# Optimization experiments

Measured on AMD Instinct MI355X. Metric: run time of the kernel, lower is better.

The kernel has to match this reference:

```python
import jax, jax.numpy as jnp
import numpy as np

N_NODES = 100000


def gcn_conv(x, W, b, src, dst):
    """PyG-style GCNConv: symmetric normalization with self-loops.
    x: [N, Cin], W: [Cin, Cout], b: [Cout], src/dst: [E] int (messages src->dst)."""
    N = x.shape[0]
    h = x @ W  # [N, Cout]
    # degree with self-loops (fill_value = 1)
    deg = jnp.ones((N,), dtype=x.dtype).at[dst].add(1.0)
    d_inv = jax.lax.rsqrt(deg)
    norm = d_inv[src] * d_inv[dst]  # [E]
    msg = h[src] * norm[:, None]  # [E, Cout] -- dominant memory traffic
    agg = jnp.zeros_like(h).at[dst].add(msg)
    # self-loop contribution: norm_ii = d_inv[i]^2
    agg = agg + h * (d_inv * d_inv)[:, None]
    return agg + b


def setup_inputs() -> dict:
    key = jax.random.key(0)
    k1, k2, k3, k4 = jax.random.split(key, 4)
    N, E, Cin, Chid, Cout = N_NODES, 1600000, 128, 128, 64
    x = jax.random.normal(k1, (N, Cin), dtype=jnp.float32)
    edge_index = jax.random.randint(k2, (2, E), 0, N, dtype=jnp.int32)
    W1 = jax.random.normal(k3, (Cin, Chid), dtype=jnp.float32) / np.sqrt(Cin)
    b1 = jnp.zeros((Chid,), dtype=jnp.float32)
    W2 = jax.random.normal(k4, (Chid, Cout), dtype=jnp.float32) / np.sqrt(Chid)
    b2 = jnp.zeros((Cout,), dtype=jnp.float32)
    return {"x": x, "edge_index": edge_index, "W1": W1, "b1": b1, "W2": W2, "b2": b2}


def reference(x, edge_index, W1, b1, W2, b2):
    src, dst = edge_index[0], edge_index[1]
    h = jax.nn.relu(gcn_conv(x, W1, b1, src, dst))  # conv1: in -> 2*out
    z = jax.nn.relu(gcn_conv(h, W2, b2, src, dst))  # conv2: 2*out -> out
    return z
```

## Files before the change

### kernel.cpp

```cpp
#include <hip/hip_runtime.h>
#include <hip/hip_fp16.h>

#define TPB 256
#define CAP 32
#define OVFCAP 65536

typedef __attribute__((ext_vector_type(8))) short bf16x8;
typedef __attribute__((ext_vector_type(4))) float f32x4;

__device__ inline void split1(float x, unsigned short& h, unsigned short& l) {
  unsigned xb = __float_as_uint(x);
  h = (unsigned short)(xb >> 16);
  float hf = __uint_as_float(xb & 0xFFFF0000u);
  float lf = x - hf;
  l = (unsigned short)(__float_as_uint(lf) >> 16);
}

__device__ inline void split4(const float4 v, ushort4& h, ushort4& l) {
  split1(v.x, h.x, l.x);
  split1(v.y, h.y, l.y);
  split1(v.z, h.z, l.z);
  split1(v.w, h.w, l.w);
}

__global__ void k_fillslot(const int* __restrict__ src, const int* __restrict__ dst,
                           int* __restrict__ cnt, int* __restrict__ col2,
                           uint2* __restrict__ ovf, int* __restrict__ ovfn,
                           int E, int N) {
  const int g = blockIdx.x & 7;
  const int gb = blockIdx.x >> 3;
  const int gstride = (gridDim.x >> 3) * blockDim.x;
  const int lo = (int)(((long long)g * N) >> 3);
  const int hi = (int)(((long long)(g + 1) * N) >> 3);
  for (int e = gb * blockDim.x + threadIdx.x; e < E; e += gstride) {
    int d = __builtin_nontemporal_load(dst + e);
    if (d >= lo && d < hi) {
      int s = __builtin_nontemporal_load(src + e);
      int c = atomicAdd(cnt + d, 1);
      if (c < CAP) {
        col2[(size_t)d * CAP + c] = s;
      } else {
        int p = atomicAdd(ovfn, 1);
        if (p < OVFCAP) ovf[p] = make_uint2((unsigned)d, (unsigned)s);
      }
    }
  }
}

__global__ void k_dinv_from_cnt(const int* __restrict__ cnt, float* __restrict__ dinv, int N) {
  int i = blockIdx.x * blockDim.x + threadIdx.x;
  if (i < N) dinv[i] = rsqrtf((float)(cnt[i] + 1));
}

__global__ void k_prep_wt2(const float* __restrict__ W1, unsigned short* __restrict__ W1h,
                           unsigned short* __restrict__ W1l, int K1, int C1,
                           const float* __restrict__ W2, unsigned short* __restrict__ W2h,
                           unsigned short* __restrict__ W2l, int K2, int C2) {
  int i = blockIdx.x * blockDim.x + threadIdx.x;
  int n1 = K1 * C1;
  if (i < n1) {
    int k = i / C1, c = i % C1;
    unsigned short h, l;
    split1(W1[i], h, l);
    W1h[(size_t)c * K1 + k] = h;
    W1l[(size_t)c * K1 + k] = l;
  } else if (i < n1 + K2 * C2) {
    int ii = i - n1;
    int k = ii / C2, c = ii % C2;
    unsigned short h, l;
    split1(W2[ii], h, l);
    W2h[(size_t)c * K2 + k] = h;
    W2l[(size_t)c * K2 + k] = l;
  }
}

template<int COUT>
__launch_bounds__(512)
__global__ void k_gemm_mfma(const float* __restrict__ X, const unsigned short* __restrict__ Wh,
                            const unsigned short* __restrict__ Wl, const float* __restrict__ dinv,
                            __half* __restrict__ Y16, int N) {
  constexpr int K = 128;
  constexpr int BM = 128;
  constexpr int WCOL = COUT / 2;
  constexpr int NFRAG = WCOL / 16;
  __shared__ unsigned short Ah[BM * K], Al[BM * K];
  __shared__ unsigned short Wsh[COUT * K], Wsl[COUT * K];

  const int tid = threadIdx.x;
  const int rb = blockIdx.x * BM;

  {
    const uint4* gh = (const uint4*)Wh;
    const uint4* gl = (const uint4*)Wl;
    for (int i = tid; i < COUT * 16; i += 512) {
      int r = i >> 4, c = i & 15;
      int byte = r * 256 + ((c * 16) ^ ((r & 7) << 4));
      *(uint4*)((char*)Wsh + byte) = gh[i];
      *(uint4*)((char*)Wsl + byte) = gl[i];
    }
  }
  {
    for (int i = tid; i < BM * 32; i += 512) {
      int r = i >> 5, c4 = i & 31;
      int g = rb + r;
      if (g < N) {
        float4 v = ((const float4*)(X + (size_t)g * K))[c4];
        ushort4 h, l;
        split4(v, h, l);
        int byte = r * 256 + ((c4 * 8) ^ ((r & 7) << 4));
        *(ushort4*)((char*)Ah + byte) = h;
        *(ushort4*)((char*)Al + byte) = l;
      }
    }
  }
  __syncthreads();

  const int wid = tid >> 6, lane = tid & 63;
  const int wm = wid & 3;
  const int wn = wid >> 2;
  const int RB = wm * 32;
  const int CB = wn * WCOL;
  const int l15 = lane & 15, l4 = lane >> 4;
  const int xs = (l15 & 7) << 4;

  f32x4 acc[2][NFRAG];
  #pragma unroll
  for (int m = 0; m < 2; ++m)
    #pragma unroll
    for (int n = 0; n < NFRAG; ++n)
      acc[m][n] = (f32x4){0.f, 0.f, 0.f, 0.f};

  #pragma unroll
  for (int ks = 0; ks < 4; ++ks) {
    const int cbx = (ks * 64 + l4 * 16) ^ xs;
    bf16x8 a0h = *(const bf16x8*)((const char*)Ah + (RB + l15) * 256 + cbx);
    bf16x8 a0l = *(const bf16x8*)((const char*)Al + (RB + l15) * 256 + cbx);
    bf16x8 a1h = *(const bf16x8*)((const char*)Ah + (RB + 16 + l15) * 256 + cbx);
    bf16x8 a1l = *(const bf16x8*)((const char*)Al + (RB + 16 + l15) * 256 + cbx);
    #pragma unroll
    for (int n = 0; n < NFRAG; ++n) {
      const int wr = CB + n * 16 + l15;
      bf16x8 bh = *(const bf16x8*)((const char*)Wsh + wr * 256 + cbx);
      bf16x8 bl = *(const bf16x8*)((const char*)Wsl + wr * 256 + cbx);
      acc[0][n] = __builtin_amdgcn_mfma_f32_16x16x32_bf16(a0h, bh, acc[0][n], 0, 0, 0);
      acc[0][n] = __builtin_amdgcn_mfma_f32_16x16x32_bf16(a0h, bl, acc[0][n], 0, 0, 0);
      acc[0][n] = __builtin_amdgcn_mfma_f32_16x16x32_bf16(a0l, bh, acc[0][n], 0, 0, 0);
      acc[1][n] = __builtin_amdgcn_mfma_f32_16x16x32_bf16(a1h, bh, acc[1][n], 0, 0, 0);
      acc[1][n] = __builtin_amdgcn_mfma_f32_16x16x32_bf16(a1h, bl, acc[1][n], 0, 0, 0);
      acc[1][n] = __builtin_amdgcn_mfma_f32_16x16x32_bf16(a1l, bh, acc[1][n], 0, 0, 0);
    }
  }

  #pragma unroll
  for (int m = 0; m < 2; ++m) {
    #pragma unroll
    for (int q = 0; q < 4; ++q) {
      int row = rb + RB + m * 16 + l4 * 4 + q;
      if (row < N) {
        float dv = dinv[row];
        __half* yr = Y16 + (size_t)row * COUT + CB + l15;
        #pragma unroll
        for (int n = 0; n < NFRAG; ++n) yr[n * 16] = __float2half(acc[m][n][q] * dv);
      }
    }
  }
}

template<int C>
__launch_bounds__(256)
__global__ void k_aggv(const __half* __restrict__ hsh, const float* __restrict__ dinv,
                       const int* __restrict__ cnt, const int* __restrict__ col2,
                       const uint2* __restrict__ ovf, const int* __restrict__ ovfn,
                       const float* __restrict__ bias, float* __restrict__ out, int N) {
  constexpr int LPR = C / 8;
  constexpr int NG = 64 / LPR;
  constexpr int SPR = 4 * NG;
  constexpr int NR = CAP / SPR;
  const int node = blockIdx.x * 4 + (threadIdx.x >> 6);
  if (node >= N) return;
  const int lane = threadIdx.x & 63;
  const int i = lane % LPR;
  const int j = lane / LPR;
  const int deg = cnt[node];
  const int m = min(deg, CAP);
  const int4* cp4 = (const int4*)(col2 + (size_t)node * CAP);
  const size_t coloff = (size_t)i * 8;

  float acc[8];
  #pragma unroll
  for (int q = 0; q < 8; ++q) acc[q] = 0.f;

  #pragma unroll
  for (int r = 0; r < NR; ++r) {
    if (r * SPR < m) {
      int4 idx = cp4[r * NG + j];
      int s0 = r * SPR + 4 * j;
      bool ok0 = s0 + 0 < m, ok1 = s0 + 1 < m, ok2 = s0 + 2 < m, ok3 = s0 + 3 < m;
      int n0 = ok0 ? idx.x : 0;
      int n1 = ok1 ? idx.y : 0;
      int n2 = ok2 ? idx.z : 0;
      int n3 = ok3 ? idx.w : 0;
      uint4 v0 = *(const uint4*)((const char*)hsh + ((size_t)n0 * C + coloff) * 2);
      uint4 v1 = *(const uint4*)((const char*)hsh + ((size_t)n1 * C + coloff) * 2);
      uint4 v2 = *(const uint4*)((const char*)hsh + ((size_t)n2 * C + coloff) * 2);
      uint4 v3 = *(const uint4*)((const char*)hsh + ((size_t)n3 * C + coloff) * 2);
      float f0 = ok0 ? 1.f : 0.f, f1 = ok1 ? 1.f : 0.f;
      float f2 = ok2 ? 1.f : 0.f, f3 = ok3 ? 1.f : 0.f;
      const __half2* h0 = (const __half2*)&v0;
      const __half2* h1 = (const __half2*)&v1;
      const __half2* h2 = (const __half2*)&v2;
      const __half2* h3 = (const __half2*)&v3;
      #pragma unroll
      for (int q = 0; q < 4; ++q) {
        float2 a = __half22float2(h0[q]);
        float2 b = __half22float2(h1[q]);
        float2 c = __half22float2(h2[q]);
        float2 d = __half22float2(h3[q]);
        acc[2 * q]     = fmaf(f0, a.x, acc[2 * q]);
        acc[2 * q + 1] = fmaf(f0, a.y, acc[2 * q + 1]);
        acc[2 * q]     = fmaf(f1, b.x, acc[2 * q]);
        acc[2 * q + 1] = fmaf(f1, b.y, acc[2 * q + 1]);
        acc[2 * q]     = fmaf(f2, c.x, acc[2 * q]);
        acc[2 * q + 1] = fmaf(f2, c.y, acc[2 * q + 1]);
        acc[2 * q]     = fmaf(f3, d.x, acc[2 * q]);
        acc[2 * q + 1] = fmaf(f3, d.y, acc[2 * q + 1]);
      }
    }
  }

  if (deg > CAP && j == 0) {
    int on = min(*ovfn, (int)OVFCAP);
    for (int k = 0; k < on; ++k) {
      uint2 eo = ovf[k];
      if ((int)eo.x == node) {
        uint4 v = *(const uint4*)((const char*)hsh + ((size_t)eo.y * C + coloff) * 2);
        const __half2* h2 = (const __half2*)&v;
        #pragma unroll
        for (int q = 0; q < 4; ++q) {
          float2 a = __half22float2(h2[q]);
          acc[2 * q] += a.x;
          acc[2 * q + 1] += a.y;
        }
      }
    }
  }

  #pragma unroll
  for (int off = LPR; off < 64; off <<= 1)
    #pragma unroll
    for (int q = 0; q < 8; ++q)
      acc[q] += __shfl_xor(acc[q], off);

  if (j < 2) {
    const float dv = dinv[node];
    const int f4 = 2 * i + j;
    uint2 sh = *(const uint2*)((const char*)hsh + ((size_t)node * C + (size_t)f4 * 4) * 2);
    const __half2* shh = (const __half2*)&sh;
    float2 s01 = __half22float2(shh[0]);
    float2 s23 = __half22float2(shh[1]);
    float4 bb = ((const float4*)bias)[f4];
    float4 o;
    o.x = fmaxf(fmaf(dv, s01.x + acc[4 * j + 0], bb.x), 0.f);
    o.y = fmaxf(fmaf(dv, s01.y + acc[4 * j + 1], bb.y), 0.f);
    o.z = fmaxf(fmaf(dv, s23.x + acc[4 * j + 2], bb.z), 0.f);
    o.w = fmaxf(fmaf(dv, s23.y + acc[4 * j + 3], bb.w), 0.f);
    ((float4*)(out + (size_t)node * C))[f4] = o;
  }
}

__global__ void k_fill1(float* __restrict__ p, int n) {
  int i = blockIdx.x * blockDim.x + threadIdx.x;
  if (i < n) p[i] = 1.0f;
}
__global__ void k_deg_scatter(const int* __restrict__ dst, float* __restrict__ deg, int E) {
  int e = blockIdx.x * blockDim.x + threadIdx.x;
  if (e < E) atomicAdd(deg + dst[e], 1.0f);
}
__global__ void k_rsqrt_inplace(float* __restrict__ p, int n) {
  int i = blockIdx.x * blockDim.x + threadIdx.x;
  if (i < n) p[i] = rsqrtf(p[i]);
}
template<int COUT>
__launch_bounds__(256)
__global__ void k_gemm128(const float* __restrict__ X, const float* __restrict__ W,
                          const float* __restrict__ dinv, float* __restrict__ Y, int N) {
  constexpr int K = 128;
  constexpr int CG = COUT / 8;
  constexpr int ROWS = 256 / CG;
  constexpr int XSTR = K + 4;
  __shared__ float Ws[K * COUT];
  __shared__ float Xs[ROWS * XSTR];
  const int tid = threadIdx.x;

  const float4* W4 = (const float4*)W;
  float4* Ws4 = (float4*)Ws;
  #pragma unroll
  for (int i = tid; i < K * COUT / 4; i += 256) Ws4[i] = W4[i];

  const int rb = blockIdx.x * ROWS;
  float4* Xs4 = (float4*)Xs;
  for (int i = tid; i < ROWS * (K / 4); i += 256) {
    int r = i / (K / 4), c = i % (K / 4);
    float4 v = make_float4(0.f, 0.f, 0.f, 0.f);
    if (rb + r < N) v = ((const float4*)(X + (size_t)(rb + r) * K))[c];
    Xs4[r * (XSTR / 4) + c] = v;
  }
  __syncthreads();

  const int lrow = tid / CG;
  const int cg = tid % CG;
  const int row = rb + lrow;
  float acc[8];
  #pragma unroll
  for (int jj = 0; jj < 8; ++jj) acc[jj] = 0.f;
  const float* xr = Xs + lrow * XSTR;
  #pragma unroll 4
  for (int k = 0; k < K; ++k) {
    float xv = xr[k];
    float4 w0 = Ws4[k * (COUT / 4) + cg * 2];
    float4 w1 = Ws4[k * (COUT / 4) + cg * 2 + 1];
    acc[0] = fmaf(xv, w0.x, acc[0]);
    acc[1] = fmaf(xv, w0.y, acc[1]);
    acc[2] = fmaf(xv, w0.z, acc[2]);
    acc[3] = fmaf(xv, w0.w, acc[3]);
    acc[4] = fmaf(xv, w1.x, acc[4]);
    acc[5] = fmaf(xv, w1.y, acc[5]);
    acc[6] = fmaf(xv, w1.z, acc[6]);
    acc[7] = fmaf(xv, w1.w, acc[7]);
  }
  if (row < N) {
    float ds = dinv[row];
    float4* y = (float4*)(Y + (size_t)row * COUT + cg * 8);
    y[0] = make_float4(acc[0] * ds, acc[1] * ds, acc[2] * ds, acc[3] * ds);
    y[1] = make_float4(acc[4] * ds, acc[5] * ds, acc[6] * ds, acc[7] * ds);
  }
}
template<int C>
__global__ void k_selfinit2(const float* __restrict__ hs, const float* __restrict__ dinv,
                            float* __restrict__ agg, int N) {
  int i = blockIdx.x * blockDim.x + threadIdx.x;
  int total = N * (C / 4);
  if (i >= total) return;
  int node = i / (C / 4);
  float di = dinv[node];
  float4 v = ((const float4*)hs)[i];
  ((float4*)agg)[i] = make_float4(v.x * di, v.y * di, v.z * di, v.w * di);
}
template<int C>
__global__ void k_scatter(const float* __restrict__ hs, const float* __restrict__ dinv,
                          const int* __restrict__ src, const int* __restrict__ dst,
                          float* __restrict__ agg, int E) {
  constexpr int LPE = C / 4;
  long long t = (long long)blockIdx.x * blockDim.x + threadIdx.x;
  int e = (int)(t / LPE);
  if (e >= E) return;
  int c4 = (int)(t % LPE);
  int s = src[e], d = dst[e];
  float nd = dinv[d];
  float4 v = ((const float4*)(hs + (size_t)s * C))[c4];
  float* a = agg + (size_t)d * C + (size_t)c4 * 4;
  atomicAdd(a + 0, v.x * nd);
  atomicAdd(a + 1, v.y * nd);
  atomicAdd(a + 2, v.z * nd);
  atomicAdd(a + 3, v.w * nd);
}
template<int C>
__global__ void k_relu_bias(const float* __restrict__ agg, const float* __restrict__ b,
                            float* __restrict__ out, int N) {
  int i = blockIdx.x * blockDim.x + threadIdx.x;
  int total = N * (C / 4);
  if (i >= total) return;
  int c4 = i % (C / 4);
  float4 bb = ((const float4*)b)[c4];
  float4 v = ((const float4*)agg)[i];
  v.x = fmaxf(v.x + bb.x, 0.f);
  v.y = fmaxf(v.y + bb.y, 0.f);
  v.z = fmaxf(v.z + bb.z, 0.f);
  v.w = fmaxf(v.w + bb.w, 0.f);
  ((float4*)out)[i] = v;
}

extern "C" void kernel_launch(void* const* d_in, const int* in_sizes, int n_in,
                              void* d_out, int out_size, void* d_ws, size_t ws_size,
                              hipStream_t stream) {
  const float* x  = (const float*)d_in[0];
  const int*   ei = (const int*)d_in[1];
  const float* W1 = (const float*)d_in[2];
  const float* b1 = (const float*)d_in[3];
  const float* W2 = (const float*)d_in[4];
  const float* b2 = (const float*)d_in[5];

  const int Cin = 128, Chid = 128, Cout2 = 64;
  const int N = in_sizes[0] / Cin;
  const int E = in_sizes[1] / 2;
  const int* src = ei;
  const int* dst = ei + E;
  float* out = (float*)d_out;
  (void)n_in; (void)out_size;

  const int nbN = (N + TPB - 1) / TPB;
  const int nbE = (E + TPB - 1) / TPB;

  auto align = [](size_t v) { return (v + 511) & ~(size_t)511; };
  char* ws = (char*)d_ws;
  size_t off = 0;
  float* dinv   = (float*)(ws + off); off += align((size_t)N * 4);
  int*   cnt    = (int*)(ws + off);   off += align((size_t)N * 4);
  unsigned short* wt1h = (unsigned short*)(ws + off); off += align((size_t)Cin * Chid * 2);
  unsigned short* wt1l = (unsigned short*)(ws + off); off += align((size_t)Cin * Chid * 2);
  unsigned short* wt2h = (unsigned short*)(ws + off); off += align((size_t)Chid * Cout2 * 2);
  unsigned short* wt2l = (unsigned short*)(ws + off); off += align((size_t)Chid * Cout2 * 2);
  int*   col2   = (int*)(ws + off);   off += align((size_t)N * CAP * 4);
  int*   ovfn   = (int*)(ws + off);   off += align((size_t)64);
  uint2* ovf    = (uint2*)(ws + off); off += align((size_t)OVFCAP * 8);
  float* B      = (float*)(ws + off); off += (size_t)N * Chid * 4;
  __half* H16   = (__half*)(ws + off); off += align((size_t)N * Chid * 2);

  const bool fast_ok = (off <= ws_size);

  if (fast_ok) {
    hipMemsetAsync(cnt, 0, (size_t)N * 4, stream);
    hipMemsetAsync(ovfn, 0, 4, stream);
    k_fillslot<<<4096, TPB, 0, stream>>>(src, dst, cnt, col2, ovf, ovfn, E, N);
    k_dinv_from_cnt<<<nbN, TPB, 0, stream>>>(cnt, dinv, N);

    {
      int total = Cin * Chid + Chid * Cout2;
      k_prep_wt2<<<(total + TPB - 1) / TPB, TPB, 0, stream>>>(
          W1, wt1h, wt1l, Cin, Chid, W2, wt2h, wt2l, Chid, Cout2);
    }

    k_gemm_mfma<128><<<(N + 127) / 128, 512, 0, stream>>>(x, wt1h, wt1l, dinv, H16, N);
    k_aggv<128><<<(N + 3) / 4, 256, 0, stream>>>(H16, dinv, cnt, col2, ovf, ovfn, b1, B, N);
    k_gemm_mfma<64><<<(N + 127) / 128, 512, 0, stream>>>(B, wt2h, wt2l, dinv, H16, N);
    k_aggv<64><<<(N + 3) / 4, 256, 0, stream>>>(H16, dinv, cnt, col2, ovf, ovfn, b2, out, N);
  } else {
    size_t o2 = 0;
    float* dinvF = (float*)(ws + o2); o2 += align((size_t)N * 4);
    float* AF = (float*)(ws + o2);    o2 += (size_t)N * Chid * 4;
    float* BF = (float*)(ws + o2);

    k_fill1<<<nbN, TPB, 0, stream>>>(dinvF, N);
    k_deg_scatter<<<nbE, TPB, 0, stream>>>(dst, dinvF, E);
    k_rsqrt_inplace<<<nbN, TPB, 0, stream>>>(dinvF, N);

    k_gemm128<128><<<(N + 15) / 16, 256, 0, stream>>>(x, W1, dinvF, AF, N);
    k_selfinit2<128><<<(N * 32 + TPB - 1) / TPB, TPB, 0, stream>>>(AF, dinvF, BF, N);
    {
      long long total = (long long)E * 32;
      k_scatter<128><<<(int)((total + TPB - 1) / TPB), TPB, 0, stream>>>(AF, dinvF, src, dst, BF, E);
    }
    k_relu_bias<128><<<(N * 32 + TPB - 1) / TPB, TPB, 0, stream>>>(BF, b1, AF, N);

    k_gemm128<64><<<(N + 31) / 32, 256, 0, stream>>>(AF, W2, dinvF, BF, N);
    k_selfinit2<64><<<(N * 16 + TPB - 1) / TPB, TPB, 0, stream>>>(BF, dinvF, out, N);
    {
      long long total = (long long)E * 16;
      k_scatter<64><<<(int)((total + TPB - 1) / TPB), TPB, 0, stream>>>(BF, dinvF, src, dst, out, E);
    }
    k_relu_bias<64><<<(N * 16 + TPB - 1) / TPB, TPB, 0, stream>>>(out, b2, out, N);
  }
}
```

Baseline: 254.6 us.

## Fuse edge slot-fill with first-layer GEMM in one heterogeneous kernel

```diff
diff --git a/kernel.cpp b/kernel.cpp
--- a/kernel.cpp
+++ b/kernel.cpp
@@ -23,25 +23,117 @@
   split1(v.w, h.w, l.w);
 }
 
-__global__ void k_fillslot(const int* __restrict__ src, const int* __restrict__ dst,
-                           int* __restrict__ cnt, int* __restrict__ col2,
-                           uint2* __restrict__ ovf, int* __restrict__ ovfn,
-                           int E, int N) {
-  const int g = blockIdx.x & 7;
-  const int gb = blockIdx.x >> 3;
-  const int gstride = (gridDim.x >> 3) * blockDim.x;
-  const int lo = (int)(((long long)g * N) >> 3);
-  const int hi = (int)(((long long)(g + 1) * N) >> 3);
-  for (int e = gb * blockDim.x + threadIdx.x; e < E; e += gstride) {
-    int d = __builtin_nontemporal_load(dst + e);
-    if (d >= lo && d < hi) {
-      int s = __builtin_nontemporal_load(src + e);
-      int c = atomicAdd(cnt + d, 1);
-      if (c < CAP) {
-        col2[(size_t)d * CAP + c] = s;
-      } else {
-        int p = atomicAdd(ovfn, 1);
-        if (p < OVFCAP) ovf[p] = make_uint2((unsigned)d, (unsigned)s);
+__launch_bounds__(512)
+__global__ void k_fused1(const float* __restrict__ X, const unsigned short* __restrict__ Wh,
+                         const unsigned short* __restrict__ Wl,
+                         const int* __restrict__ src, const int* __restrict__ dst,
+                         int* __restrict__ cnt, int* __restrict__ col2,
+                         uint2* __restrict__ ovf, int* __restrict__ ovfn,
+                         __half* __restrict__ Y16, int E, int N, int nT) {
+  constexpr int K = 128, BM = 128, COUT = 128, WCOL = 64, NFRAG = 4;
+  __shared__ unsigned short Ah[BM * K], Al[BM * K];
+  __shared__ unsigned short Wsh[COUT * K], Wsl[COUT * K];
+
+  const int grp = blockIdx.x >> 3, l8 = blockIdx.x & 7;
+
+  if (grp & 1) {
+    const int fid = (grp >> 1) * 8 + l8;
+    const int g = fid & 7, gb = fid >> 3;
+    const int gstride = 128 * 512;
+    const int lo = (int)(((long long)g * N) >> 3);
+    const int hi = (int)(((long long)(g + 1) * N) >> 3);
+    for (int e = gb * 512 + threadIdx.x; e < E; e += gstride) {
+      int d = __builtin_nontemporal_load(dst + e);
+      if (d >= lo && d < hi) {
+        int s = __builtin_nontemporal_load(src + e);
+        int c = atomicAdd(cnt + d, 1);
+        if (c < CAP) {
+          col2[(size_t)d * CAP + c] = s;
+        } else {
+          int p = atomicAdd(ovfn, 1);
+          if (p < OVFCAP) ovf[p] = make_uint2((unsigned)d, (unsigned)s);
+        }
+      }
+    }
+    return;
+  }
+
+  const int tile = (grp >> 1) * 8 + l8;
+  if (tile >= nT) return;
+  const int tid = threadIdx.x;
+  const int rb = tile * BM;
+
+  {
+    const uint4* gh = (const uint4*)Wh;
+    const uint4* gl = (const uint4*)Wl;
+    for (int i = tid; i < COUT * 16; i += 512) {
+      int r = i >> 4, c = i & 15;
+      int byte = r * 256 + ((c * 16) ^ ((r & 7) << 4));
+      *(uint4*)((char*)Wsh + byte) = gh[i];
+      *(uint4*)((char*)Wsl + byte) = gl[i];
+    }
+  }
+  {
+    for (int i = tid; i < BM * 32; i += 512) {
+      int r = i >> 5, c4 = i & 31;
+      int gr = rb + r;
+      if (gr < N) {
+        float4 v = ((const float4*)(X + (size_t)gr * K))[c4];
+        ushort4 h, l;
+        split4(v, h, l);
+        int byte = r * 256 + ((c4 * 8) ^ ((r & 7) << 4));
+        *(ushort4*)((char*)Ah + byte) = h;
+        *(ushort4*)((char*)Al + byte) = l;
+      }
+    }
+  }
+  __syncthreads();
+
+  const int wid = tid >> 6, lane = tid & 63;
+  const int wm = wid & 3;
+  const int wn = wid >> 2;
+  const int RB = wm * 32;
+  const int CB = wn * WCOL;
+  const int l15 = lane & 15, l4 = lane >> 4;
+  const int xs = (l15 & 7) << 4;
+
+  f32x4 acc[2][NFRAG];
+  #pragma unroll
+  for (int m = 0; m < 2; ++m)
+    #pragma unroll
+    for (int n = 0; n < NFRAG; ++n)
+      acc[m][n] = (f32x4){0.f, 0.f, 0.f, 0.f};
+
+  #pragma unroll
+  for (int ks = 0; ks < 4; ++ks) {
+    const int cbx = (ks * 64 + l4 * 16) ^ xs;
+    bf16x8 a0h = *(const bf16x8*)((const char*)Ah + (RB + l15) * 256 + cbx);
+    bf16x8 a0l = *(const bf16x8*)((const char*)Al + (RB + l15) * 256 + cbx);
+    bf16x8 a1h = *(const bf16x8*)((const char*)Ah + (RB + 16 + l15) * 256 + cbx);
+    bf16x8 a1l = *(const bf16x8*)((const char*)Al + (RB + 16 + l15) * 256 + cbx);
+    #pragma unroll
+    for (int n = 0; n < NFRAG; ++n) {
+      const int wr = CB + n * 16 + l15;
+      bf16x8 bh = *(const bf16x8*)((const char*)Wsh + wr * 256 + cbx);
+      bf16x8 bl = *(const bf16x8*)((const char*)Wsl + wr * 256 + cbx);
+      acc[0][n] = __builtin_amdgcn_mfma_f32_16x16x32_bf16(a0h, bh, acc[0][n], 0, 0, 0);
+      acc[0][n] = __builtin_amdgcn_mfma_f32_16x16x32_bf16(a0h, bl, acc[0][n], 0, 0, 0);
+      acc[0][n] = __builtin_amdgcn_mfma_f32_16x16x32_bf16(a0l, bh, acc[0][n], 0, 0, 0);
+      acc[1][n] = __builtin_amdgcn_mfma_f32_16x16x32_bf16(a1h, bh, acc[1][n], 0, 0, 0);
+      acc[1][n] = __builtin_amdgcn_mfma_f32_16x16x32_bf16(a1h, bl, acc[1][n], 0, 0, 0);
+      acc[1][n] = __builtin_amdgcn_mfma_f32_16x16x32_bf16(a1l, bh, acc[1][n], 0, 0, 0);
+    }
+  }
+
+  #pragma unroll
+  for (int m = 0; m < 2; ++m) {
+    #pragma unroll
+    for (int q = 0; q < 4; ++q) {
+      int row = rb + RB + m * 16 + l4 * 4 + q;
+      if (row < N) {
+        __half* yr = Y16 + (size_t)row * COUT + CB + l15;
+        #pragma unroll
+        for (int n = 0; n < NFRAG; ++n) yr[n * 16] = __float2half(acc[m][n][q]);
       }
     }
   }
@@ -50,6 +142,22 @@
 __global__ void k_dinv_from_cnt(const int* __restrict__ cnt, float* __restrict__ dinv, int N) {
   int i = blockIdx.x * blockDim.x + threadIdx.x;
   if (i < N) dinv[i] = rsqrtf((float)(cnt[i] + 1));
+}
+
+__global__ void k_scale16(__half* __restrict__ H, const float* __restrict__ dinv, int total16) {
+  int i = blockIdx.x * blockDim.x + threadIdx.x;
+  if (i >= total16) return;
+  float dv = dinv[i >> 4];
+  uint4* p = (uint4*)H + i;
+  uint4 v = *p;
+  __half2* h2 = (__half2*)&v;
+  #pragma unroll
+  for (int q = 0; q < 4; ++q) {
+    float2 f = __half22float2(h2[q]);
+    f.x *= dv; f.y *= dv;
+    h2[q] = __float22half2_rn(f);
+  }
+  *p = v;
 }
 
 __global__ void k_prep_wt2(const float* __restrict__ W1, unsigned short* __restrict__ W1h,
@@ -400,6 +508,7 @@
 
   const int nbN = (N + TPB - 1) / TPB;
   const int nbE = (E + TPB - 1) / TPB;
+  const int nT = (N + 127) / 128;
 
   auto align = [](size_t v) { return (v + 511) & ~(size_t)511; };
   char* ws = (char*)d_ws;
@@ -416,21 +525,23 @@
   float* B      = (float*)(ws + off); off += (size_t)N * Chid * 4;
   __half* H16   = (__half*)(ws + off); off += align((size_t)N * Chid * 2);
 
-  const bool fast_ok = (off <= ws_size);
+  const bool fast_ok = (off <= ws_size) && (nT <= 1024);
 
   if (fast_ok) {
     hipMemsetAsync(cnt, 0, (size_t)N * 4, stream);
     hipMemsetAsync(ovfn, 0, 4, stream);
-    k_fillslot<<<4096, TPB, 0, stream>>>(src, dst, cnt, col2, ovf, ovfn, E, N);
-    k_dinv_from_cnt<<<nbN, TPB, 0, stream>>>(cnt, dinv, N);
-
     {
       int total = Cin * Chid + Chid * Cout2;
       k_prep_wt2<<<(total + TPB - 1) / TPB, TPB, 0, stream>>>(
           W1, wt1h, wt1l, Cin, Chid, W2, wt2h, wt2l, Chid, Cout2);
     }
 
-    k_gemm_mfma<128><<<(N + 127) / 128, 512, 0, stream>>>(x, wt1h, wt1l, dinv, H16, N);
+    k_fused1<<<2048, 512, 0, stream>>>(x, wt1h, wt1l, src, dst, cnt, col2, ovf, ovfn,
+                                       H16, E, N, nT);
+
+    k_dinv_from_cnt<<<nbN, TPB, 0, stream>>>(cnt, dinv, N);
+    k_scale16<<<(N * 16 + TPB - 1) / TPB, TPB, 0, stream>>>(H16, dinv, N * 16);
+
     k_aggv<128><<<(N + 3) / 4, 256, 0, stream>>>(H16, dinv, cnt, col2, ovf, ovfn, b1, B, N);
     k_gemm_mfma<64><<<(N + 127) / 128, 512, 0, stream>>>(B, wt2h, wt2l, dinv, H16, N);
     k_aggv<64><<<(N + 3) / 4, 256, 0, stream>>>(H16, dinv, cnt, col2, ovf, ovfn, b2, out, N);
```

New measurement: 386.1 us. 51.6% more time.
